# Kernel optimization log

Hardware: AMD Instinct MI355X
Metric: run time of the kernel (lower is better)

The kernel has to match this reference:

```python
import jax, jax.numpy as jnp
import numpy as np

N_NODES = 100000
N_EDGES = 1600000
K = 3  # TAGConv default hops


def _make_lin(key, out_dim, in_dim):
    # K+1 bias-free linears (stacked) + one shared output bias, per PyG TAGConv
    kw, = jax.random.split(key, 1)
    scale = 1.0 / np.sqrt(in_dim)
    W = jax.random.uniform(kw, (K + 1, out_dim, in_dim), jnp.float32, -scale, scale)
    b = jnp.zeros((out_dim,), jnp.float32)
    return W, b


def setup_inputs() -> dict:
    key = jax.random.key(0)
    ks = jax.random.split(key, 6)
    x = jax.random.normal(ks[0], (N_NODES, 128), jnp.float32)
    edge_index = jax.random.randint(ks[1], (2, N_EDGES), 0, N_NODES, jnp.int64)
    W1, b1 = _make_lin(ks[2], 128, 128)
    W2, b2 = _make_lin(ks[3], 64, 128)
    W3, b3 = _make_lin(ks[4], 16, 64)
    return {"x": x, "edge_index": edge_index, "W1": W1, "b1": b1,
            "W2": W2, "b2": b2, "W3": W3, "b3": b3}


def _tagconv(x, row, col, norm, W, b, n):
    # out = sum_k lin_k(A_norm^k x) + b ; message x_j*norm gathered at col
    out = jnp.einsum('nd,od->no', x, W[0])
    h = x
    for k in range(1, W.shape[0]):
        h = jax.ops.segment_sum(norm[:, None] * h[row], col, num_segments=n)
        out = out + jnp.einsum('nd,od->no', h, W[k])
    return out + b


def _dropout(x, key, p=0.5):
    keep = jax.random.bernoulli(key, 1.0 - p, x.shape)
    return jnp.where(keep, x / (1.0 - p), 0.0)


def reference(x, edge_index, W1, b1, W2, b2, W3, b3):
    n = x.shape[0]
    row, col = edge_index[0], edge_index[1]
    # gcn_norm without self-loops (TAGConv default)
    deg = jax.ops.segment_sum(jnp.ones(row.shape[0], x.dtype), col, num_segments=n)
    dis = jnp.where(deg > 0, 1.0 / jnp.sqrt(jnp.where(deg > 0, deg, 1.0)), 0.0)
    norm = dis[row] * dis[col]

    dk1, dk2 = jax.random.split(jax.random.key(42))
    h = _tagconv(x, row, col, norm, W1, b1, n)
    h = _dropout(h, dk1)
    h = _tagconv(h, row, col, norm, W2, b2, n)
    h = jax.nn.elu(h)
    h = _dropout(h, dk2)
    h = _tagconv(h, row, col, norm, W3, b3, n)
    return h
```

## Files before the change

### kernel.cpp

```cpp
#include <hip/hip_runtime.h>
#include <stdint.h>
#include <math.h>

#define N_NODES 100000
#define N_EDGES 1600000

typedef __bf16 bf16_t;
typedef __attribute__((ext_vector_type(4))) __bf16 bf16x4;
typedef __attribute__((ext_vector_type(8))) __bf16 bf16x8;
typedef __attribute__((ext_vector_type(4))) float f32x4;

__device__ __forceinline__ f32x4 mfma16(bf16x8 a, bf16x8 b, f32x4 c) {
  return __builtin_amdgcn_mfma_f32_16x16x32_bf16(a, b, c, 0, 0, 0);
}

__device__ __host__ __forceinline__ uint32_t rotl32(uint32_t v, int d) {
  return (v << d) | (v >> (32 - d));
}

__device__ __host__ __forceinline__ void threefry2x32(uint32_t k0, uint32_t k1,
                                                      uint32_t x0, uint32_t x1,
                                                      uint32_t& o0, uint32_t& o1) {
  uint32_t ks0 = k0, ks1 = k1, ks2 = k0 ^ k1 ^ 0x1BD11BDAu;
  x0 += ks0; x1 += ks1;
#define TF_R(r) { x0 += x1; x1 = rotl32(x1, r); x1 ^= x0; }
  TF_R(13) TF_R(15) TF_R(26) TF_R(6)
  x0 += ks1; x1 += ks2 + 1u;
  TF_R(17) TF_R(29) TF_R(16) TF_R(24)
  x0 += ks2; x1 += ks0 + 2u;
  TF_R(13) TF_R(15) TF_R(26) TF_R(6)
  x0 += ks0; x1 += ks1 + 3u;
  TF_R(17) TF_R(29) TF_R(16) TF_R(24)
  x0 += ks1; x1 += ks2 + 4u;
  TF_R(13) TF_R(15) TF_R(26) TF_R(6)
  x0 += ks2; x1 += ks0 + 5u;
#undef TF_R
  o0 = x0; o1 = x1;
}

__device__ __forceinline__ float drop_scale(uint32_t idx, uint32_t k0, uint32_t k1) {
  uint32_t o0, o1;
  threefry2x32(k0, k1, 0u, idx, o0, o1);
  uint32_t bits = o0 ^ o1;
  float u = __uint_as_float((bits >> 9) | 0x3f800000u) - 1.0f;
  return (u < 0.5f) ? 2.0f : 0.0f;
}

__global__ __launch_bounds__(256) void detect_kernel(const int* __restrict__ ei,
                                                     int* __restrict__ found_nonzero) {
  int idx = blockIdx.x * 256 + threadIdx.x;
  size_t j = (size_t)idx * 781;
  if (ei[2 * j + 1] != 0) atomicOr(found_nonzero, 1);
}

__device__ __forceinline__ int edge_row(const int* ei, bool i32, int e) {
  return i32 ? ei[e] : ei[2 * (size_t)e];
}
__device__ __forceinline__ int edge_col(const int* ei, bool i32, int e) {
  return i32 ? ei[N_EDGES + e] : ei[2 * ((size_t)N_EDGES + (size_t)e)];
}

#define BKT_SHIFT 8
#define NBKT 391
#define BKT_CAP 6144
#define EPB 8192
#define NBLK 196
#define SCAN_M (NBKT * NBLK)

__global__ __launch_bounds__(256) void hist_kernel(const int* __restrict__ ei,
                                                   const int* __restrict__ flag,
                                                   int* __restrict__ hist) {
  __shared__ int h[NBKT];
  const int t = threadIdx.x, blk = blockIdx.x;
  for (int i = t; i < NBKT; i += 256) h[i] = 0;
  __syncthreads();
  const bool i32 = *flag != 0;
  const int e0 = blk * EPB;
  for (int i = t; i < EPB; i += 256) {
    int e = e0 + i;
    if (e < N_EDGES) atomicAdd(&h[edge_col(ei, i32, e) >> BKT_SHIFT], 1);
  }
  __syncthreads();
  for (int i = t; i < NBKT; i += 256) hist[i * NBLK + blk] = h[i];
}

__global__ __launch_bounds__(256) void btot_kernel(const int* __restrict__ hist,
                                                   int* __restrict__ btot) {
  __shared__ int sh[256];
  const int b = blockIdx.x, t = threadIdx.x;
  int s = 0;
  for (int i = t; i < NBLK; i += 256) s += hist[b * NBLK + i];
  sh[t] = s;
  __syncthreads();
  for (int ofs = 128; ofs > 0; ofs >>= 1) {
    if (t < ofs) sh[t] += sh[t + ofs];
    __syncthreads();
  }
  if (t == 0) btot[b] = sh[0];
}

__global__ __launch_bounds__(512) void bbase_kernel(const int* __restrict__ btot,
                                                    int* __restrict__ bbase,
                                                    int* __restrict__ S) {
  __shared__ int sh[512];
  const int t = threadIdx.x;
  int v = (t < NBKT) ? btot[t] : 0;
  sh[t] = v;
  __syncthreads();
  for (int ofs = 1; ofs < 512; ofs <<= 1) {
    int u = (t >= ofs) ? sh[t - ofs] : 0;
    __syncthreads();
    sh[t] += u;
    __syncthreads();
  }
  if (t < NBKT) bbase[t] = sh[t] - v;
  if (t == 0) S[SCAN_M] = N_EDGES;
}

__global__ __launch_bounds__(256) void bscan2_kernel(const int* __restrict__ hist,
                                                     const int* __restrict__ bbase,
                                                     int* __restrict__ S) {
  __shared__ int sh[256];
  const int b = blockIdx.x, t = threadIdx.x;
  int v = (t < NBLK) ? hist[b * NBLK + t] : 0;
  sh[t] = v;
  __syncthreads();
  for (int ofs = 1; ofs < 256; ofs <<= 1) {
    int u = (t >= ofs) ? sh[t - ofs] : 0;
    __syncthreads();
    sh[t] += u;
    __syncthreads();
  }
  if (t < NBLK) S[b * NBLK + t] = bbase[b] + sh[t] - v;
}

__global__ __launch_bounds__(256) void binfill_kernel(const int* __restrict__ ei,
                                                      const int* __restrict__ flag,
                                                      const int* __restrict__ S,
                                                      int2* __restrict__ bins) {
  __shared__ int cur[NBKT];
  const int t = threadIdx.x, blk = blockIdx.x;
  for (int i = t; i < NBKT; i += 256) cur[i] = S[i * NBLK + blk];
  __syncthreads();
  const bool i32 = *flag != 0;
  const int e0 = blk * EPB;
  for (int i = t; i < EPB; i += 256) {
    int e = e0 + i;
    if (e < N_EDGES) {
      int r = edge_row(ei, i32, e);
      int c = edge_col(ei, i32, e);
      int p = atomicAdd(&cur[c >> BKT_SHIFT], 1);
      bins[p] = make_int2(r, c);
    }
  }
}

__global__ __launch_bounds__(512) void degdis_kernel(const int2* __restrict__ bins,
                                                     const int* __restrict__ S,
                                                     float* __restrict__ dis,
                                                     int* __restrict__ rptr) {
  __shared__ int h[256];
  __shared__ int sc[256];
  const int b = blockIdx.x, t = threadIdx.x;
  const int Bb = S[b * NBLK];
  const int Be = S[(b + 1) * NBLK];
  if (t < 256) h[t] = 0;
  __syncthreads();
  for (int i = t; i < Be - Bb; i += 512)
    atomicAdd(&h[bins[Bb + i].y & 255], 1);
  __syncthreads();
  if (t < 256) sc[t] = h[t];
  __syncthreads();
  for (int ofs = 1; ofs < 256; ofs <<= 1) {
    int u = 0;
    if (t >= ofs && t < 256) u = sc[t - ofs];
    __syncthreads();
    if (t < 256) sc[t] += u;
    __syncthreads();
  }
  const int c0 = b << BKT_SHIFT;
  if (t < 256 && c0 + t < N_NODES) {
    int d = h[t];
    dis[c0 + t] = (d > 0) ? (1.0f / sqrtf((float)d)) : 0.0f;
    rptr[c0 + t] = Bb + sc[t] - d;
  }
  if (b == NBKT - 1 && t == 0) rptr[N_NODES] = N_EDGES;
}

__global__ __launch_bounds__(512) void scatter_kernel(
    const int2* __restrict__ bins, const float* __restrict__ dis,
    const int* __restrict__ rptr, int2* __restrict__ erec) {
  __shared__ int loff[256];
  __shared__ int lcur[256];
  __shared__ float ldis[256];
  __shared__ int2 stage[BKT_CAP];
  const int b = blockIdx.x;
  const int c0 = b << BKT_SHIFT;
  const int nn = min(256, N_NODES - c0);
  const int t = threadIdx.x;
  const int base = rptr[c0];
  if (t < nn) {
    loff[t] = rptr[c0 + t] - base;
    lcur[t] = 0;
    ldis[t] = dis[c0 + t];
  }
  __syncthreads();
  const int cnt = min(rptr[c0 + nn] - base, BKT_CAP);
  for (int i = t; i < cnt; i += 512) {
    int2 rec = bins[base + i];
    int lc = rec.y & 255;
    float nrm = dis[rec.x] * ldis[lc];
    int p = atomicAdd(&lcur[lc], 1);
    stage[loff[lc] + p] = make_int2(rec.x, __float_as_int(nrm));
  }
  __syncthreads();
  for (int i = t; i < cnt; i += 512) erec[base + i] = stage[i];
}

__global__ __launch_bounds__(256) void wcvt_kernel(
    const float* __restrict__ W1, const float* __restrict__ W2,
    const float* __restrict__ W3,
    bf16_t* __restrict__ Wb1, bf16_t* __restrict__ Wb2,
    bf16_t* __restrict__ Wb3) {
  int i = blockIdx.x * 256 + threadIdx.x;
  if (i < 65536) Wb1[i] = (bf16_t)W1[i];
  if (i < 32768) Wb2[i] = (bf16_t)W2[i];
  if (i < 4096)  Wb3[i] = (bf16_t)W3[i];
}

template <int DIN, int LOG_DOUT, int NCH, bool YB, bool AHL>
__global__ __launch_bounds__(256) void matmul_mfma_kernel(
    const void* __restrict__ hA, const void* __restrict__ hAlo,
    const bf16_t* __restrict__ Wb, const float* __restrict__ bias,
    float* __restrict__ y0, void* __restrict__ y1,
    void* __restrict__ y2, void* __restrict__ y3) {
  constexpr int LDK = DIN + 8;
  constexpr int DOUT = 1 << LOG_DOUT;
  constexpr int KI = DIN / 32;
  __shared__ bf16_t sm[2][64 * LDK];
  const int m0 = blockIdx.x * 64;
  const int tid = threadIdx.x;

  if (AHL) {
    constexpr int NL = 64 * DIN / 8 / 256;
#pragma unroll
    for (int it = 0; it < NL; ++it) {
      int idx = tid + it * 256;
      int r = idx / (DIN / 8), cc = (idx % (DIN / 8)) * 8;
      int gm = m0 + r;
      uint4 vh = make_uint4(0, 0, 0, 0), vl = make_uint4(0, 0, 0, 0);
      if (gm < N_NODES) {
        vh = ((const uint4*)hA)[((size_t)gm * DIN + cc) >> 3];
        vl = ((const uint4*)hAlo)[((size_t)gm * DIN + cc) >> 3];
      }
      *(uint4*)&sm[0][r * LDK + cc] = vh;
      *(uint4*)&sm[1][r * LDK + cc] = vl;
    }
  } else {
    constexpr int NL = 64 * DIN / 4 / 256;
    union U4 { bf16_t b[4]; uint2 u; };
#pragma unroll
    for (int it = 0; it < NL; ++it) {
      int idx = tid + it * 256;
      int r = idx / (DIN / 4), cc = (idx % (DIN / 4)) * 4;
      int gm = m0 + r;
      float4 v = (gm < N_NODES) ? ((const float4*)hA)[((size_t)gm * DIN + cc) >> 2]
                                : make_float4(0.f, 0.f, 0.f, 0.f);
      U4 hi, lo;
      hi.b[0] = (bf16_t)v.x; lo.b[0] = (bf16_t)(v.x - (float)hi.b[0]);
      hi.b[1] = (bf16_t)v.y; lo.b[1] = (bf16_t)(v.y - (float)hi.b[1]);
      hi.b[2] = (bf16_t)v.z; lo.b[2] = (bf16_t)(v.z - (float)hi.b[2]);
      hi.b[3] = (bf16_t)v.w; lo.b[3] = (bf16_t)(v.w - (float)hi.b[3]);
      *(uint2*)&sm[0][r * LDK + cc] = hi.u;
      *(uint2*)&sm[1][r * LDK + cc] = lo.u;
    }
  }
  __syncthreads();

  const int w = tid >> 6, lane = tid & 63;
  const int wm = w & 1, wn = w >> 1;
  const int quad = lane >> 4, lr = lane & 15;

  bf16x8 aH[2][KI], aL[2][KI];
#pragma unroll
  for (int mt = 0; mt < 2; ++mt)
#pragma unroll
    for (int ki = 0; ki < KI; ++ki) {
      int rowa = wm * 32 + mt * 16 + lr;
      int koff = ki * 32 + quad * 8;
      aH[mt][ki] = *(const bf16x8*)&sm[0][rowa * LDK + koff];
      aL[mt][ki] = *(const bf16x8*)&sm[1][rowa * LDK + koff];
    }
  __syncthreads();

  constexpr int NLB = 64 * DIN / 8 / 256;
  uint4 wreg[NLB];
#pragma unroll
  for (int it = 0; it < NLB; ++it) {
    int idx = tid + it * 256;
    int r = idx / (DIN / 8), cc = (idx % (DIN / 8)) * 8;
    wreg[it] = ((const uint4*)Wb)[(((size_t)r) * DIN + cc) >> 3];
    *(uint4*)&sm[0][r * LDK + cc] = wreg[it];
  }
  __syncthreads();

  for (int nc = 0; nc < NCH; ++nc) {
    int p = nc & 1;
    if (nc + 1 < NCH) {
#pragma unroll
      for (int it = 0; it < NLB; ++it) {
        int idx = tid + it * 256;
        int r = idx / (DIN / 8), cc = (idx % (DIN / 8)) * 8;
        wreg[it] = ((const uint4*)Wb)[(((size_t)((nc + 1) * 64 + r)) * DIN + cc) >> 3];
      }
    }

    f32x4 acc[2][2] = {};
#pragma unroll
    for (int ki = 0; ki < KI; ++ki) {
      int koff = ki * 32 + quad * 8;
      bf16x8 bfr[2];
#pragma unroll
      for (int nt = 0; nt < 2; ++nt)
        bfr[nt] = *(const bf16x8*)&sm[p][(wn * 32 + nt * 16 + lr) * LDK + koff];
#pragma unroll
      for (int mt = 0; mt < 2; ++mt)
#pragma unroll
        for (int nt = 0; nt < 2; ++nt) {
          acc[mt][nt] = mfma16(bfr[nt], aH[mt][ki], acc[mt][nt]);
          acc[mt][nt] = mfma16(bfr[nt], aL[mt][ki], acc[mt][nt]);
        }
    }

    if (nc + 1 < NCH) {
#pragma unroll
      for (int it = 0; it < NLB; ++it) {
        int idx = tid + it * 256;
        int r = idx / (DIN / 8), cc = (idx % (DIN / 8)) * 8;
        *(uint4*)&sm[p ^ 1][r * LDK + cc] = wreg[it];
      }
    }
    __syncthreads();

    const int n0 = nc * 64;
#pragma unroll
    for (int mt = 0; mt < 2; ++mt) {
      int m = m0 + wm * 32 + mt * 16 + lr;
      if (m >= N_NODES) continue;
#pragma unroll
      for (int nt = 0; nt < 2; ++nt) {
        int nb = n0 + wn * 32 + nt * 16 + quad * 4;
        int k = nb >> LOG_DOUT;
        int o = nb & (DOUT - 1);
        size_t oi = (size_t)m * DOUT + o;
        if (k == 0) {
          float4 bv = *(const float4*)&bias[o];
          float4 st = make_float4(acc[mt][nt][0] + bv.x, acc[mt][nt][1] + bv.y,
                                  acc[mt][nt][2] + bv.z, acc[mt][nt][3] + bv.w);
          *(float4*)&y0[oi] = st;
        } else {
          void* yk = (k == 1) ? y1 : (k == 2) ? y2 : y3;
          if (YB) {
            bf16x4 bb;
            bb.x = (bf16_t)acc[mt][nt][0];
            bb.y = (bf16_t)acc[mt][nt][1];
            bb.z = (bf16_t)acc[mt][nt][2];
            bb.w = (bf16_t)acc[mt][nt][3];
            *(bf16x4*)((bf16_t*)yk + oi) = bb;
          } else {
            *(f32x4*)((float*)yk + oi) = acc[mt][nt];
          }
        }
      }
    }
  }
}

template <int D, int EPI, bool ZBF, bool ABF, int OMODE>
__global__ __launch_bounds__(256) void prop_kernel(
    const void* __restrict__ zv, const void* __restrict__ addv,
    void* __restrict__ outv, void* __restrict__ outv2,
    const int* __restrict__ rptr, const int2* __restrict__ erec,
    uint32_t k0, uint32_t k1) {
  constexpr int LPN = D / 4;
  constexpr int NPB = 256 / LPN;
  int lane = threadIdx.x % LPN;
  int nsub = threadIdx.x / LPN;
  int c = blockIdx.x * NPB + nsub;
  if (c >= N_NODES) return;
  int e0 = rptr[c], e1 = rptr[c + 1];
  float a0 = 0.f, a1 = 0.f, a2 = 0.f, a3 = 0.f;

  auto ld = [&](int r, float v[4]) {
    if (ZBF) {
      bf16x4 t = ((const bf16x4*)zv)[(size_t)r * LPN + lane];
      v[0] = (float)t.x; v[1] = (float)t.y; v[2] = (float)t.z; v[3] = (float)t.w;
    } else {
      float4 t = ((const float4*)zv)[(size_t)r * LPN + lane];
      v[0] = t.x; v[1] = t.y; v[2] = t.z; v[3] = t.w;
    }
  };

  int e = e0;
  for (; e + 3 < e1; e += 4) {
    int2 q[4];
    float v[4][4];
#pragma unroll
    for (int j = 0; j < 4; ++j) q[j] = erec[e + j];
#pragma unroll
    for (int j = 0; j < 4; ++j) ld(q[j].x, v[j]);
#pragma unroll
    for (int j = 0; j < 4; ++j) {
      float wv = __int_as_float(q[j].y);
      a0 = fmaf(wv, v[j][0], a0);
      a1 = fmaf(wv, v[j][1], a1);
      a2 = fmaf(wv, v[j][2], a2);
      a3 = fmaf(wv, v[j][3], a3);
    }
  }
  for (; e < e1; ++e) {
    int2 q = erec[e];
    float wv = __int_as_float(q.y);
    float v[4];
    ld(q.x, v);
    a0 = fmaf(wv, v[0], a0);
    a1 = fmaf(wv, v[1], a1);
    a2 = fmaf(wv, v[2], a2);
    a3 = fmaf(wv, v[3], a3);
  }

  size_t pidx = (size_t)c * LPN + lane;
  uint32_t fidx = (uint32_t)c * D + 4 * lane;
  float ax[4];
  if (ABF) {
    bf16x4 t = ((const bf16x4*)addv)[pidx];
    ax[0] = (float)t.x; ax[1] = (float)t.y; ax[2] = (float)t.z; ax[3] = (float)t.w;
  } else {
    float4 t = ((const float4*)addv)[pidx];
    ax[0] = t.x; ax[1] = t.y; ax[2] = t.z; ax[3] = t.w;
  }
  float o[4] = {a0 + ax[0], a1 + ax[1], a2 + ax[2], a3 + ax[3]};
  if (EPI == 1) {
#pragma unroll
    for (int j = 0; j < 4; ++j) o[j] *= drop_scale(fidx + j, k0, k1);
  }
  if (EPI == 2) {
#pragma unroll
    for (int j = 0; j < 4; ++j) {
      o[j] = (o[j] > 0.f) ? o[j] : expm1f(o[j]);
      o[j] *= drop_scale(fidx + j, k0, k1);
    }
  }
  if (OMODE == 0) {
    ((float4*)outv)[pidx] = make_float4(o[0], o[1], o[2], o[3]);
  } else if (OMODE == 1) {
    bf16x4 bv;
    bv.x = (bf16_t)o[0]; bv.y = (bf16_t)o[1];
    bv.z = (bf16_t)o[2]; bv.w = (bf16_t)o[3];
    ((bf16x4*)outv)[pidx] = bv;
  } else {
    bf16x4 hv, lv;
    hv.x = (bf16_t)o[0]; hv.y = (bf16_t)o[1];
    hv.z = (bf16_t)o[2]; hv.w = (bf16_t)o[3];
    lv.x = (bf16_t)(o[0] - (float)hv.x);
    lv.y = (bf16_t)(o[1] - (float)hv.y);
    lv.z = (bf16_t)(o[2] - (float)hv.z);
    lv.w = (bf16_t)(o[3] - (float)hv.w);
    ((bf16x4*)outv)[pidx] = hv;
    ((bf16x4*)outv2)[pidx] = lv;
  }
}

extern "C" void kernel_launch(void* const* d_in, const int* in_sizes, int n_in,
                              void* d_out, int out_size, void* d_ws, size_t ws_size,
                              hipStream_t stream) {
  const float* x  = (const float*)d_in[0];
  const int*   ei = (const int*)d_in[1];
  const float* W1 = (const float*)d_in[2];
  const float* b1 = (const float*)d_in[3];
  const float* W2 = (const float*)d_in[4];
  const float* b2 = (const float*)d_in[5];
  const float* W3 = (const float*)d_in[6];
  const float* b3 = (const float*)d_in[7];
  float* out = (float*)d_out;

  char* ws = (char*)d_ws;
  size_t off = 0;
  auto alloc = [&](size_t bytes) -> char* {
    char* p = ws + off;
    off += (bytes + 255) & ~(size_t)255;
    return p;
  };
  int*   flag   = (int*)alloc(256);
  float* dis    = (float*)alloc((size_t)N_NODES * 4);
  int*   rptr   = (int*)alloc((size_t)(N_NODES + 1) * 4);
  int*   hist   = (int*)alloc((size_t)SCAN_M * 4);
  int*   S      = (int*)alloc((size_t)(SCAN_M + 1) * 4);
  int*   btot   = (int*)alloc((size_t)NBKT * 4);
  int*   bbase  = (int*)alloc((size_t)NBKT * 4);
  int2*  erec   = (int2*)alloc((size_t)N_EDGES * 8);
  bf16_t* Wb1  = (bf16_t*)alloc(65536 * 2);
  bf16_t* Wb2  = (bf16_t*)alloc(32768 * 2);
  bf16_t* Wb3  = (bf16_t*)alloc(4096 * 2);
  float*  R0  = (float*)alloc((size_t)N_NODES * 128 * 4);
  float*  R2  = (float*)alloc((size_t)N_NODES * 16 * 4);
  bf16_t* Zb0 = (bf16_t*)alloc((size_t)N_NODES * 128 * 2);
  bf16_t* Zb1 = (bf16_t*)alloc((size_t)N_NODES * 128 * 2);
  bf16_t* Bb1 = (bf16_t*)alloc((size_t)N_NODES * 128 * 2);
  bf16_t* Bb2 = (bf16_t*)alloc((size_t)N_NODES * 128 * 2);

  int2* bins = (int2*)R0;

  hipMemsetAsync(flag, 0, 256, stream);

  detect_kernel<<<8, 256, 0, stream>>>(ei, flag);
  hist_kernel<<<NBLK, 256, 0, stream>>>(ei, flag, hist);
  btot_kernel<<<NBKT, 256, 0, stream>>>(hist, btot);
  bbase_kernel<<<1, 512, 0, stream>>>(btot, bbase, S);
  bscan2_kernel<<<NBKT, 256, 0, stream>>>(hist, bbase, S);
  binfill_kernel<<<NBLK, 256, 0, stream>>>(ei, flag, S, bins);
  degdis_kernel<<<NBKT, 512, 0, stream>>>(bins, S, dis, rptr);
  scatter_kernel<<<NBKT, 512, 0, stream>>>(bins, dis, rptr, erec);
  wcvt_kernel<<<256, 256, 0, stream>>>(W1, W2, W3, Wb1, Wb2, Wb3);

  uint32_t d10, d11, d20, d21;
  threefry2x32(0u, 42u, 0u, 0u, d10, d11);
  threefry2x32(0u, 42u, 0u, 1u, d20, d21);

  const int MB = (N_NODES + 63) / 64;
  const int PB128 = (N_NODES + 7) / 8;
  const int PB64n = (N_NODES + 15) / 16;
  const int PB16n = (N_NODES + 63) / 64;

  matmul_mfma_kernel<128, 7, 8, true, false><<<MB, 256, 0, stream>>>(
      x, nullptr, Wb1, b1, R0, Bb1, Bb2, Zb0);
  prop_kernel<128, 0, true, true, 1><<<PB128, 256, 0, stream>>>(
      Zb0, Bb2, Zb1, nullptr, rptr, erec, 0, 0);
  prop_kernel<128, 0, true, true, 1><<<PB128, 256, 0, stream>>>(
      Zb1, Bb1, Zb0, nullptr, rptr, erec, 0, 0);
  prop_kernel<128, 1, true, false, 2><<<PB128, 256, 0, stream>>>(
      Zb0, R0, Bb2, Bb1, rptr, erec, d10, d11);

  float*  R1f = R0;
  bf16_t* S0 = Zb0;
  bf16_t* S1 = Zb0 + (size_t)N_NODES * 64;
  bf16_t* S2 = Zb1;
  bf16_t* S3 = Zb1 + (size_t)N_NODES * 64;
  matmul_mfma_kernel<128, 6, 4, true, true><<<MB, 256, 0, stream>>>(
      Bb2, Bb1, Wb2, b2, R1f, S2, S3, S0);
  prop_kernel<64, 0, true, true, 1><<<PB64n, 256, 0, stream>>>(
      S0, S3, S1, nullptr, rptr, erec, 0, 0);
  prop_kernel<64, 0, true, true, 1><<<PB64n, 256, 0, stream>>>(
      S1, S2, S0, nullptr, rptr, erec, 0, 0);
  prop_kernel<64, 2, true, false, 2><<<PB64n, 256, 0, stream>>>(
      S0, R1f, S2, S3, rptr, erec, d20, d21);

  float*  z0f = R2;
  bf16_t* zb1 = Bb1;
  bf16_t* zb2 = Bb1 + (size_t)N_NODES * 16;
  bf16_t* zb3 = Bb1 + (size_t)N_NODES * 32;
  matmul_mfma_kernel<64, 4, 1, true, true><<<MB, 256, 0, stream>>>(
      S2, S3, Wb3, b3, z0f, zb1, zb2, zb3);
  prop_kernel<16, 0, true, true, 1><<<PB16n, 256, 0, stream>>>(
      zb3, zb2, zb2, nullptr, rptr, erec, 0, 0);
  prop_kernel<16, 0, true, true, 1><<<PB16n, 256, 0, stream>>>(
      zb2, zb1, zb1, nullptr, rptr, erec, 0, 0);
  prop_kernel<16, 0, true, false, 0><<<PB16n, 256, 0, stream>>>(
      zb1, z0f, out, nullptr, rptr, erec, 0, 0);

  (void)in_sizes; (void)n_in; (void)out_size; (void)ws_size;
}
```

Baseline: 656.8 us.

## Slice node features into 16-column planes so each XCD gathers one L2-resident slice

Stores node feature arrays as 16-column slices laid out contiguously across all nodes. The matmul writes and reads in this layout, and the propagation kernel maps blockIdx&7 to a feature slice. Since blocks are dispatched round-robin across XCDs, each XCD should repeatedly gather from a single slice of about 3.2 MB that can stay in its L2. Edge records shrink to a 4-byte source index, and the normalization is rebuilt from dis at use time, which saves CSR bandwidth. The cost is re-reading the edge list and dis once per slice, and making narrower 32-byte gathers.

Result: slower. 999.4 us (+52.2%).

```diff
diff --git a/kernel.cpp b/kernel.cpp
--- a/kernel.cpp
+++ b/kernel.cpp
@@ -188,12 +188,11 @@
 }
 
 __global__ __launch_bounds__(512) void scatter_kernel(
-    const int2* __restrict__ bins, const float* __restrict__ dis,
-    const int* __restrict__ rptr, int2* __restrict__ erec) {
+    const int2* __restrict__ bins, const int* __restrict__ rptr,
+    uint32_t* __restrict__ erow) {
   __shared__ int loff[256];
   __shared__ int lcur[256];
-  __shared__ float ldis[256];
-  __shared__ int2 stage[BKT_CAP];
+  __shared__ uint32_t stage[BKT_CAP];
   const int b = blockIdx.x;
   const int c0 = b << BKT_SHIFT;
   const int nn = min(256, N_NODES - c0);
@@ -202,19 +201,17 @@
   if (t < nn) {
     loff[t] = rptr[c0 + t] - base;
     lcur[t] = 0;
-    ldis[t] = dis[c0 + t];
   }
   __syncthreads();
   const int cnt = min(rptr[c0 + nn] - base, BKT_CAP);
   for (int i = t; i < cnt; i += 512) {
     int2 rec = bins[base + i];
     int lc = rec.y & 255;
-    float nrm = dis[rec.x] * ldis[lc];
     int p = atomicAdd(&lcur[lc], 1);
-    stage[loff[lc] + p] = make_int2(rec.x, __float_as_int(nrm));
-  }
-  __syncthreads();
-  for (int i = t; i < cnt; i += 512) erec[base + i] = stage[i];
+    stage[loff[lc] + p] = (uint32_t)rec.x;
+  }
+  __syncthreads();
+  for (int i = t; i < cnt; i += 512) erow[base + i] = stage[i];
 }
 
 __global__ __launch_bounds__(256) void wcvt_kernel(
@@ -250,8 +247,10 @@
       int gm = m0 + r;
       uint4 vh = make_uint4(0, 0, 0, 0), vl = make_uint4(0, 0, 0, 0);
       if (gm < N_NODES) {
-        vh = ((const uint4*)hA)[((size_t)gm * DIN + cc) >> 3];
-        vl = ((const uint4*)hAlo)[((size_t)gm * DIN + cc) >> 3];
+        size_t go = ((size_t)(cc >> 4) * N_NODES * 16 + (size_t)gm * 16 +
+                     (cc & 15)) >> 3;
+        vh = ((const uint4*)hA)[go];
+        vl = ((const uint4*)hAlo)[go];
       }
       *(uint4*)&sm[0][r * LDK + cc] = vh;
       *(uint4*)&sm[1][r * LDK + cc] = vl;
@@ -352,7 +351,8 @@
         int nb = n0 + wn * 32 + nt * 16 + quad * 4;
         int k = nb >> LOG_DOUT;
         int o = nb & (DOUT - 1);
-        size_t oi = (size_t)m * DOUT + o;
+        size_t oi = (size_t)(o >> 4) * ((size_t)N_NODES * 16) +
+                    (size_t)m * 16 + (o & 15);
         if (k == 0) {
           float4 bv = *(const float4*)&bias[o];
           float4 st = make_float4(acc[mt][nt][0] + bv.x, acc[mt][nt][1] + bv.y,
@@ -376,98 +376,96 @@
   }
 }
 
-template <int D, int EPI, bool ZBF, bool ABF, int OMODE>
+template <int NSL, int EPI, bool ABF, int OMODE>
 __global__ __launch_bounds__(256) void prop_kernel(
-    const void* __restrict__ zv, const void* __restrict__ addv,
+    const bf16_t* __restrict__ zv, const void* __restrict__ addv,
     void* __restrict__ outv, void* __restrict__ outv2,
-    const int* __restrict__ rptr, const int2* __restrict__ erec,
-    uint32_t k0, uint32_t k1) {
-  constexpr int LPN = D / 4;
-  constexpr int NPB = 256 / LPN;
-  int lane = threadIdx.x % LPN;
-  int nsub = threadIdx.x / LPN;
-  int c = blockIdx.x * NPB + nsub;
+    const int* __restrict__ rptr, const uint32_t* __restrict__ erow,
+    const float* __restrict__ dis, uint32_t k0, uint32_t k1) {
+  constexpr int D = NSL * 16;
+  constexpr int NREP = 8 / NSL;
+  const int v = blockIdx.x & 7;
+  const int s = v & (NSL - 1);
+  const int chunk = (blockIdx.x >> 3) * NREP + (v / NSL);
+  const int lane = threadIdx.x & 1;
+  const int nsub = threadIdx.x >> 1;
+  const int c = chunk * 128 + nsub;
   if (c >= N_NODES) return;
-  int e0 = rptr[c], e1 = rptr[c + 1];
-  float a0 = 0.f, a1 = 0.f, a2 = 0.f, a3 = 0.f;
-
-  auto ld = [&](int r, float v[4]) {
-    if (ZBF) {
-      bf16x4 t = ((const bf16x4*)zv)[(size_t)r * LPN + lane];
-      v[0] = (float)t.x; v[1] = (float)t.y; v[2] = (float)t.z; v[3] = (float)t.w;
-    } else {
-      float4 t = ((const float4*)zv)[(size_t)r * LPN + lane];
-      v[0] = t.x; v[1] = t.y; v[2] = t.z; v[3] = t.w;
-    }
-  };
+  const bf16x8* zs = (const bf16x8*)(zv + (size_t)s * N_NODES * 16);
+  const int e0 = rptr[c], e1 = rptr[c + 1];
+  const float dc = dis[c];
+  float a[8] = {};
 
   int e = e0;
   for (; e + 3 < e1; e += 4) {
-    int2 q[4];
-    float v[4][4];
-#pragma unroll
-    for (int j = 0; j < 4; ++j) q[j] = erec[e + j];
-#pragma unroll
-    for (int j = 0; j < 4; ++j) ld(q[j].x, v[j]);
+    uint32_t r4[4];
+    float w4[4];
+    bf16x8 t4[4];
+#pragma unroll
+    for (int j = 0; j < 4; ++j) r4[j] = erow[e + j];
 #pragma unroll
     for (int j = 0; j < 4; ++j) {
-      float wv = __int_as_float(q[j].y);
-      a0 = fmaf(wv, v[j][0], a0);
-      a1 = fmaf(wv, v[j][1], a1);
-      a2 = fmaf(wv, v[j][2], a2);
-      a3 = fmaf(wv, v[j][3], a3);
+      w4[j] = dis[r4[j]];
+      t4[j] = zs[(size_t)r4[j] * 2 + lane];
+    }
+#pragma unroll
+    for (int j = 0; j < 4; ++j) {
+      float w = w4[j] * dc;
+#pragma unroll
+      for (int q = 0; q < 8; ++q) a[q] = fmaf(w, (float)t4[j][q], a[q]);
     }
   }
   for (; e < e1; ++e) {
-    int2 q = erec[e];
-    float wv = __int_as_float(q.y);
-    float v[4];
-    ld(q.x, v);
-    a0 = fmaf(wv, v[0], a0);
-    a1 = fmaf(wv, v[1], a1);
-    a2 = fmaf(wv, v[2], a2);
-    a3 = fmaf(wv, v[3], a3);
-  }
-
-  size_t pidx = (size_t)c * LPN + lane;
-  uint32_t fidx = (uint32_t)c * D + 4 * lane;
-  float ax[4];
+    uint32_t r = erow[e];
+    float w = dis[r] * dc;
+    bf16x8 t = zs[(size_t)r * 2 + lane];
+#pragma unroll
+    for (int q = 0; q < 8; ++q) a[q] = fmaf(w, (float)t[q], a[q]);
+  }
+
+  const size_t pidx = (size_t)s * N_NODES * 2 + (size_t)c * 2 + lane;
+  const size_t fidx4 = ((size_t)s * N_NODES * 16 + (size_t)c * 16 + lane * 8) >> 2;
+  float o[8];
   if (ABF) {
-    bf16x4 t = ((const bf16x4*)addv)[pidx];
-    ax[0] = (float)t.x; ax[1] = (float)t.y; ax[2] = (float)t.z; ax[3] = (float)t.w;
+    bf16x8 t = ((const bf16x8*)addv)[pidx];
+#pragma unroll
+    for (int q = 0; q < 8; ++q) o[q] = a[q] + (float)t[q];
   } else {
-    float4 t = ((const float4*)addv)[pidx];
-    ax[0] = t.x; ax[1] = t.y; ax[2] = t.z; ax[3] = t.w;
-  }
-  float o[4] = {a0 + ax[0], a1 + ax[1], a2 + ax[2], a3 + ax[3]};
+    const float4* af = (const float4*)addv;
+    float4 t0 = af[fidx4], t1 = af[fidx4 + 1];
+    o[0] = a[0] + t0.x; o[1] = a[1] + t0.y; o[2] = a[2] + t0.z; o[3] = a[3] + t0.w;
+    o[4] = a[4] + t1.x; o[5] = a[5] + t1.y; o[6] = a[6] + t1.z; o[7] = a[7] + t1.w;
+  }
+  const uint32_t fidx = (uint32_t)c * D + (uint32_t)(s * 16 + lane * 8);
   if (EPI == 1) {
 #pragma unroll
-    for (int j = 0; j < 4; ++j) o[j] *= drop_scale(fidx + j, k0, k1);
+    for (int q = 0; q < 8; ++q) o[q] *= drop_scale(fidx + q, k0, k1);
   }
   if (EPI == 2) {
 #pragma unroll
-    for (int j = 0; j < 4; ++j) {
-      o[j] = (o[j] > 0.f) ? o[j] : expm1f(o[j]);
-      o[j] *= drop_scale(fidx + j, k0, k1);
+    for (int q = 0; q < 8; ++q) {
+      o[q] = (o[q] > 0.f) ? o[q] : expm1f(o[q]);
+      o[q] *= drop_scale(fidx + q, k0, k1);
     }
   }
   if (OMODE == 0) {
-    ((float4*)outv)[pidx] = make_float4(o[0], o[1], o[2], o[3]);
+    float4* of = (float4*)outv;
+    of[fidx4] = make_float4(o[0], o[1], o[2], o[3]);
+    of[fidx4 + 1] = make_float4(o[4], o[5], o[6], o[7]);
   } else if (OMODE == 1) {
-    bf16x4 bv;
-    bv.x = (bf16_t)o[0]; bv.y = (bf16_t)o[1];
-    bv.z = (bf16_t)o[2]; bv.w = (bf16_t)o[3];
-    ((bf16x4*)outv)[pidx] = bv;
+    bf16x8 bv;
+#pragma unroll
+    for (int q = 0; q < 8; ++q) bv[q] = (bf16_t)o[q];
+    ((bf16x8*)outv)[pidx] = bv;
   } else {
-    bf16x4 hv, lv;
-    hv.x = (bf16_t)o[0]; hv.y = (bf16_t)o[1];
-    hv.z = (bf16_t)o[2]; hv.w = (bf16_t)o[3];
-    lv.x = (bf16_t)(o[0] - (float)hv.x);
-    lv.y = (bf16_t)(o[1] - (float)hv.y);
-    lv.z = (bf16_t)(o[2] - (float)hv.z);
-    lv.w = (bf16_t)(o[3] - (float)hv.w);
-    ((bf16x4*)outv)[pidx] = hv;
-    ((bf16x4*)outv2)[pidx] = lv;
+    bf16x8 hv, lv;
+#pragma unroll
+    for (int q = 0; q < 8; ++q) {
+      hv[q] = (bf16_t)o[q];
+      lv[q] = (bf16_t)(o[q] - (float)hv[q]);
+    }
+    ((bf16x8*)outv)[pidx] = hv;
+    ((bf16x8*)outv2)[pidx] = lv;
   }
 }
 
@@ -498,7 +496,7 @@
   int*   S      = (int*)alloc((size_t)(SCAN_M + 1) * 4);
   int*   btot   = (int*)alloc((size_t)NBKT * 4);
   int*   bbase  = (int*)alloc((size_t)NBKT * 4);
-  int2*  erec   = (int2*)alloc((size_t)N_EDGES * 8);
+  uint32_t* erow = (uint32_t*)alloc((size_t)N_EDGES * 4);
   bf16_t* Wb1  = (bf16_t*)alloc(65536 * 2);
   bf16_t* Wb2  = (bf16_t*)alloc(32768 * 2);
   bf16_t* Wb3  = (bf16_t*)alloc(4096 * 2);
@@ -520,7 +518,7 @@
   bscan2_kernel<<<NBKT, 256, 0, stream>>>(hist, bbase, S);
   binfill_kernel<<<NBLK, 256, 0, stream>>>(ei, flag, S, bins);
   degdis_kernel<<<NBKT, 512, 0, stream>>>(bins, S, dis, rptr);
-  scatter_kernel<<<NBKT, 512, 0, stream>>>(bins, dis, rptr, erec);
+  scatter_kernel<<<NBKT, 512, 0, stream>>>(bins, rptr, erow);
   wcvt_kernel<<<256, 256, 0, stream>>>(W1, W2, W3, Wb1, Wb2, Wb3);
 
   uint32_t d10, d11, d20, d21;
@@ -528,18 +526,19 @@
   threefry2x32(0u, 42u, 0u, 1u, d20, d21);
 
   const int MB = (N_NODES + 63) / 64;
-  const int PB128 = (N_NODES + 7) / 8;
-  const int PB64n = (N_NODES + 15) / 16;
-  const int PB16n = (N_NODES + 63) / 64;
+  const int NCH = (N_NODES + 127) / 128;
+  const int PG8 = 8 * NCH;
+  const int PG4 = 8 * ((NCH + 1) / 2);
+  const int PG1 = 8 * ((NCH + 7) / 8);
 
   matmul_mfma_kernel<128, 7, 8, true, false><<<MB, 256, 0, stream>>>(
       x, nullptr, Wb1, b1, R0, Bb1, Bb2, Zb0);
-  prop_kernel<128, 0, true, true, 1><<<PB128, 256, 0, stream>>>(
-      Zb0, Bb2, Zb1, nullptr, rptr, erec, 0, 0);
-  prop_kernel<128, 0, true, true, 1><<<PB128, 256, 0, stream>>>(
-      Zb1, Bb1, Zb0, nullptr, rptr, erec, 0, 0);
-  prop_kernel<128, 1, true, false, 2><<<PB128, 256, 0, stream>>>(
-      Zb0, R0, Bb2, Bb1, rptr, erec, d10, d11);
+  prop_kernel<8, 0, true, 1><<<PG8, 256, 0, stream>>>(
+      Zb0, Bb2, Zb1, nullptr, rptr, erow, dis, 0, 0);
+  prop_kernel<8, 0, true, 1><<<PG8, 256, 0, stream>>>(
+      Zb1, Bb1, Zb0, nullptr, rptr, erow, dis, 0, 0);
+  prop_kernel<8, 1, false, 2><<<PG8, 256, 0, stream>>>(
+      Zb0, R0, Bb2, Bb1, rptr, erow, dis, d10, d11);
 
   float*  R1f = R0;
   bf16_t* S0 = Zb0;
@@ -548,12 +547,12 @@
   bf16_t* S3 = Zb1 + (size_t)N_NODES * 64;
   matmul_mfma_kernel<128, 6, 4, true, true><<<MB, 256, 0, stream>>>(
       Bb2, Bb1, Wb2, b2, R1f, S2, S3, S0);
-  prop_kernel<64, 0, true, true, 1><<<PB64n, 256, 0, stream>>>(
-      S0, S3, S1, nullptr, rptr, erec, 0, 0);
-  prop_kernel<64, 0, true, true, 1><<<PB64n, 256, 0, stream>>>(
-      S1, S2, S0, nullptr, rptr, erec, 0, 0);
-  prop_kernel<64, 2, true, false, 2><<<PB64n, 256, 0, stream>>>(
-      S0, R1f, S2, S3, rptr, erec, d20, d21);
+  prop_kernel<4, 0, true, 1><<<PG4, 256, 0, stream>>>(
+      S0, S3, S1, nullptr, rptr, erow, dis, 0, 0);
+  prop_kernel<4, 0, true, 1><<<PG4, 256, 0, stream>>>(
+      S1, S2, S0, nullptr, rptr, erow, dis, 0, 0);
+  prop_kernel<4, 2, false, 2><<<PG4, 256, 0, stream>>>(
+      S0, R1f, S2, S3, rptr, erow, dis, d20, d21);
 
   float*  z0f = R2;
   bf16_t* zb1 = Bb1;
@@ -561,12 +560,12 @@
   bf16_t* zb3 = Bb1 + (size_t)N_NODES * 32;
   matmul_mfma_kernel<64, 4, 1, true, true><<<MB, 256, 0, stream>>>(
       S2, S3, Wb3, b3, z0f, zb1, zb2, zb3);
-  prop_kernel<16, 0, true, true, 1><<<PB16n, 256, 0, stream>>>(
-      zb3, zb2, zb2, nullptr, rptr, erec, 0, 0);
-  prop_kernel<16, 0, true, true, 1><<<PB16n, 256, 0, stream>>>(
-      zb2, zb1, zb1, nullptr, rptr, erec, 0, 0);
-  prop_kernel<16, 0, true, false, 0><<<PB16n, 256, 0, stream>>>(
-      zb1, z0f, out, nullptr, rptr, erec, 0, 0);
+  prop_kernel<1, 0, true, 1><<<PG1, 256, 0, stream>>>(
+      zb3, zb2, zb2, nullptr, rptr, erow, dis, 0, 0);
+  prop_kernel<1, 0, true, 1><<<PG1, 256, 0, stream>>>(
+      zb2, zb1, zb1, nullptr, rptr, erow, dis, 0, 0);
+  prop_kernel<1, 0, false, 0><<<PG1, 256, 0, stream>>>(
+      zb1, z0f, out, nullptr, rptr, erow, dis, 0, 0);
 
   (void)in_sizes; (void)n_in; (void)out_size; (void)ws_size;
 }
```

## Store row-only edge list and compute edge norm on the fly in propagation

Applied to the files above, without the earlier changes.

Replaces the 8-byte (row, norm) edge records with 4-byte row indices and recomputes the weight as dis[row]*dis[col] inside each propagation kernel. The degree and scatter kernels are fused into one, which drops a launch and a pass over the bins. The propagation gather loop is unrolled to 8 edges, with a 4-edge step before the scalar tail. This halves edge-stream bandwidth across nine propagation passes, at the cost of an extra random gather into dis per edge (a small 400KB array, likely cache-resident).

Result: no change. 648.8 us (-1.2%).

```diff
diff --git a/kernel.cpp b/kernel.cpp
--- a/kernel.cpp
+++ b/kernel.cpp
@@ -155,18 +155,22 @@
   }
 }
 
-__global__ __launch_bounds__(512) void degdis_kernel(const int2* __restrict__ bins,
-                                                     const int* __restrict__ S,
-                                                     float* __restrict__ dis,
-                                                     int* __restrict__ rptr) {
+__global__ __launch_bounds__(512) void degdis_scatter_kernel(
+    const int2* __restrict__ bins, const int* __restrict__ S,
+    float* __restrict__ dis, int* __restrict__ rptr,
+    uint32_t* __restrict__ erow) {
   __shared__ int h[256];
   __shared__ int sc[256];
+  __shared__ int loff[256];
+  __shared__ int lcur[256];
+  __shared__ uint32_t reord[BKT_CAP];
   const int b = blockIdx.x, t = threadIdx.x;
   const int Bb = S[b * NBLK];
   const int Be = S[(b + 1) * NBLK];
+  const int cnt = min(Be - Bb, BKT_CAP);
   if (t < 256) h[t] = 0;
   __syncthreads();
-  for (int i = t; i < Be - Bb; i += 512)
+  for (int i = t; i < cnt; i += 512)
     atomicAdd(&h[bins[Bb + i].y & 255], 1);
   __syncthreads();
   if (t < 256) sc[t] = h[t];
@@ -179,42 +183,25 @@
     __syncthreads();
   }
   const int c0 = b << BKT_SHIFT;
-  if (t < 256 && c0 + t < N_NODES) {
-    int d = h[t];
-    dis[c0 + t] = (d > 0) ? (1.0f / sqrtf((float)d)) : 0.0f;
-    rptr[c0 + t] = Bb + sc[t] - d;
+  if (t < 256) {
+    loff[t] = sc[t] - h[t];
+    lcur[t] = 0;
+    if (c0 + t < N_NODES) {
+      int d = h[t];
+      dis[c0 + t] = (d > 0) ? (1.0f / sqrtf((float)d)) : 0.0f;
+      rptr[c0 + t] = Bb + sc[t] - d;
+    }
   }
   if (b == NBKT - 1 && t == 0) rptr[N_NODES] = N_EDGES;
-}
-
-__global__ __launch_bounds__(512) void scatter_kernel(
-    const int2* __restrict__ bins, const float* __restrict__ dis,
-    const int* __restrict__ rptr, int2* __restrict__ erec) {
-  __shared__ int loff[256];
-  __shared__ int lcur[256];
-  __shared__ float ldis[256];
-  __shared__ int2 stage[BKT_CAP];
-  const int b = blockIdx.x;
-  const int c0 = b << BKT_SHIFT;
-  const int nn = min(256, N_NODES - c0);
-  const int t = threadIdx.x;
-  const int base = rptr[c0];
-  if (t < nn) {
-    loff[t] = rptr[c0 + t] - base;
-    lcur[t] = 0;
-    ldis[t] = dis[c0 + t];
-  }
-  __syncthreads();
-  const int cnt = min(rptr[c0 + nn] - base, BKT_CAP);
+  __syncthreads();
   for (int i = t; i < cnt; i += 512) {
-    int2 rec = bins[base + i];
+    int2 rec = bins[Bb + i];
     int lc = rec.y & 255;
-    float nrm = dis[rec.x] * ldis[lc];
     int p = atomicAdd(&lcur[lc], 1);
-    stage[loff[lc] + p] = make_int2(rec.x, __float_as_int(nrm));
-  }
-  __syncthreads();
-  for (int i = t; i < cnt; i += 512) erec[base + i] = stage[i];
+    reord[loff[lc] + p] = (uint32_t)rec.x;
+  }
+  __syncthreads();
+  for (int i = t; i < cnt; i += 512) erow[Bb + i] = reord[i];
 }
 
 __global__ __launch_bounds__(256) void wcvt_kernel(
@@ -376,61 +363,77 @@
   }
 }
 
-template <int D, int EPI, bool ZBF, bool ABF, int OMODE>
+template <int D, int EPI, bool ABF, int OMODE>
 __global__ __launch_bounds__(256) void prop_kernel(
-    const void* __restrict__ zv, const void* __restrict__ addv,
+    const bf16_t* __restrict__ zv, const void* __restrict__ addv,
     void* __restrict__ outv, void* __restrict__ outv2,
-    const int* __restrict__ rptr, const int2* __restrict__ erec,
-    uint32_t k0, uint32_t k1) {
+    const int* __restrict__ rptr, const uint32_t* __restrict__ erow,
+    const float* __restrict__ dis, uint32_t k0, uint32_t k1) {
   constexpr int LPN = D / 4;
   constexpr int NPB = 256 / LPN;
-  int lane = threadIdx.x % LPN;
-  int nsub = threadIdx.x / LPN;
-  int c = blockIdx.x * NPB + nsub;
+  const int lane = threadIdx.x % LPN;
+  const int nsub = threadIdx.x / LPN;
+  const int c = blockIdx.x * NPB + nsub;
   if (c >= N_NODES) return;
-  int e0 = rptr[c], e1 = rptr[c + 1];
+  const int e0 = rptr[c], e1 = rptr[c + 1];
+  const float dc = dis[c];
+  const bf16x4* zs = (const bf16x4*)zv;
   float a0 = 0.f, a1 = 0.f, a2 = 0.f, a3 = 0.f;
 
-  auto ld = [&](int r, float v[4]) {
-    if (ZBF) {
-      bf16x4 t = ((const bf16x4*)zv)[(size_t)r * LPN + lane];
-      v[0] = (float)t.x; v[1] = (float)t.y; v[2] = (float)t.z; v[3] = (float)t.w;
-    } else {
-      float4 t = ((const float4*)zv)[(size_t)r * LPN + lane];
-      v[0] = t.x; v[1] = t.y; v[2] = t.z; v[3] = t.w;
-    }
-  };
-
   int e = e0;
-  for (; e + 3 < e1; e += 4) {
-    int2 q[4];
-    float v[4][4];
-#pragma unroll
-    for (int j = 0; j < 4; ++j) q[j] = erec[e + j];
-#pragma unroll
-    for (int j = 0; j < 4; ++j) ld(q[j].x, v[j]);
+  for (; e + 7 < e1; e += 8) {
+    uint32_t r8[8];
+#pragma unroll
+    for (int j = 0; j < 8; ++j) r8[j] = erow[e + j];
+    float w8[8];
+    bf16x4 v8[8];
+#pragma unroll
+    for (int j = 0; j < 8; ++j) {
+      w8[j] = dis[r8[j]];
+      v8[j] = zs[(size_t)r8[j] * LPN + lane];
+    }
+#pragma unroll
+    for (int j = 0; j < 8; ++j) {
+      float w = w8[j] * dc;
+      a0 = fmaf(w, (float)v8[j].x, a0);
+      a1 = fmaf(w, (float)v8[j].y, a1);
+      a2 = fmaf(w, (float)v8[j].z, a2);
+      a3 = fmaf(w, (float)v8[j].w, a3);
+    }
+  }
+  if (e + 3 < e1) {
+    uint32_t r4[4];
+#pragma unroll
+    for (int j = 0; j < 4; ++j) r4[j] = erow[e + j];
+    float w4[4];
+    bf16x4 v4[4];
 #pragma unroll
     for (int j = 0; j < 4; ++j) {
-      float wv = __int_as_float(q[j].y);
-      a0 = fmaf(wv, v[j][0], a0);
-      a1 = fmaf(wv, v[j][1], a1);
-      a2 = fmaf(wv, v[j][2], a2);
-      a3 = fmaf(wv, v[j][3], a3);
-    }
+      w4[j] = dis[r4[j]];
+      v4[j] = zs[(size_t)r4[j] * LPN + lane];
+    }
+#pragma unroll
+    for (int j = 0; j < 4; ++j) {
+      float w = w4[j] * dc;
+      a0 = fmaf(w, (float)v4[j].x, a0);
+      a1 = fmaf(w, (float)v4[j].y, a1);
+      a2 = fmaf(w, (float)v4[j].z, a2);
+      a3 = fmaf(w, (float)v4[j].w, a3);
+    }
+    e += 4;
   }
   for (; e < e1; ++e) {
-    int2 q = erec[e];
-    float wv = __int_as_float(q.y);
-    float v[4];
-    ld(q.x, v);
-    a0 = fmaf(wv, v[0], a0);
-    a1 = fmaf(wv, v[1], a1);
-    a2 = fmaf(wv, v[2], a2);
-    a3 = fmaf(wv, v[3], a3);
-  }
-
-  size_t pidx = (size_t)c * LPN + lane;
-  uint32_t fidx = (uint32_t)c * D + 4 * lane;
+    uint32_t r = erow[e];
+    float w = dis[r] * dc;
+    bf16x4 t = zs[(size_t)r * LPN + lane];
+    a0 = fmaf(w, (float)t.x, a0);
+    a1 = fmaf(w, (float)t.y, a1);
+    a2 = fmaf(w, (float)t.z, a2);
+    a3 = fmaf(w, (float)t.w, a3);
+  }
+
+  const size_t pidx = (size_t)c * LPN + lane;
+  const uint32_t fidx = (uint32_t)c * D + 4 * lane;
   float ax[4];
   if (ABF) {
     bf16x4 t = ((const bf16x4*)addv)[pidx];
@@ -498,7 +501,7 @@
   int*   S      = (int*)alloc((size_t)(SCAN_M + 1) * 4);
   int*   btot   = (int*)alloc((size_t)NBKT * 4);
   int*   bbase  = (int*)alloc((size_t)NBKT * 4);
-  int2*  erec   = (int2*)alloc((size_t)N_EDGES * 8);
+  uint32_t* erow = (uint32_t*)alloc((size_t)N_EDGES * 4);
   bf16_t* Wb1  = (bf16_t*)alloc(65536 * 2);
   bf16_t* Wb2  = (bf16_t*)alloc(32768 * 2);
   bf16_t* Wb3  = (bf16_t*)alloc(4096 * 2);
@@ -519,8 +522,7 @@
   bbase_kernel<<<1, 512, 0, stream>>>(btot, bbase, S);
   bscan2_kernel<<<NBKT, 256, 0, stream>>>(hist, bbase, S);
   binfill_kernel<<<NBLK, 256, 0, stream>>>(ei, flag, S, bins);
-  degdis_kernel<<<NBKT, 512, 0, stream>>>(bins, S, dis, rptr);
-  scatter_kernel<<<NBKT, 512, 0, stream>>>(bins, dis, rptr, erec);
+  degdis_scatter_kernel<<<NBKT, 512, 0, stream>>>(bins, S, dis, rptr, erow);
   wcvt_kernel<<<256, 256, 0, stream>>>(W1, W2, W3, Wb1, Wb2, Wb3);
 
   uint32_t d10, d11, d20, d21;
@@ -534,12 +536,12 @@
 
   matmul_mfma_kernel<128, 7, 8, true, false><<<MB, 256, 0, stream>>>(
       x, nullptr, Wb1, b1, R0, Bb1, Bb2, Zb0);
-  prop_kernel<128, 0, true, true, 1><<<PB128, 256, 0, stream>>>(
-      Zb0, Bb2, Zb1, nullptr, rptr, erec, 0, 0);
-  prop_kernel<128, 0, true, true, 1><<<PB128, 256, 0, stream>>>(
-      Zb1, Bb1, Zb0, nullptr, rptr, erec, 0, 0);
-  prop_kernel<128, 1, true, false, 2><<<PB128, 256, 0, stream>>>(
-      Zb0, R0, Bb2, Bb1, rptr, erec, d10, d11);
+  prop_kernel<128, 0, true, 1><<<PB128, 256, 0, stream>>>(
+      Zb0, Bb2, Zb1, nullptr, rptr, erow, dis, 0, 0);
+  prop_kernel<128, 0, true, 1><<<PB128, 256, 0, stream>>>(
+      Zb1, Bb1, Zb0, nullptr, rptr, erow, dis, 0, 0);
+  prop_kernel<128, 1, false, 2><<<PB128, 256, 0, stream>>>(
+      Zb0, R0, Bb2, Bb1, rptr, erow, dis, d10, d11);
 
   float*  R1f = R0;
   bf16_t* S0 = Zb0;
@@ -548,12 +550,12 @@
   bf16_t* S3 = Zb1 + (size_t)N_NODES * 64;
   matmul_mfma_kernel<128, 6, 4, true, true><<<MB, 256, 0, stream>>>(
       Bb2, Bb1, Wb2, b2, R1f, S2, S3, S0);
-  prop_kernel<64, 0, true, true, 1><<<PB64n, 256, 0, stream>>>(
-      S0, S3, S1, nullptr, rptr, erec, 0, 0);
-  prop_kernel<64, 0, true, true, 1><<<PB64n, 256, 0, stream>>>(
-      S1, S2, S0, nullptr, rptr, erec, 0, 0);
-  prop_kernel<64, 2, true, false, 2><<<PB64n, 256, 0, stream>>>(
-      S0, R1f, S2, S3, rptr, erec, d20, d21);
+  prop_kernel<64, 0, true, 1><<<PB64n, 256, 0, stream>>>(
+      S0, S3, S1, nullptr, rptr, erow, dis, 0, 0);
+  prop_kernel<64, 0, true, 1><<<PB64n, 256, 0, stream>>>(
+      S1, S2, S0, nullptr, rptr, erow, dis, 0, 0);
+  prop_kernel<64, 2, false, 2><<<PB64n, 256, 0, stream>>>(
+      S0, R1f, S2, S3, rptr, erow, dis, d20, d21);
 
   float*  z0f = R2;
   bf16_t* zb1 = Bb1;
@@ -561,12 +563,12 @@
   bf16_t* zb3 = Bb1 + (size_t)N_NODES * 32;
   matmul_mfma_kernel<64, 4, 1, true, true><<<MB, 256, 0, stream>>>(
       S2, S3, Wb3, b3, z0f, zb1, zb2, zb3);
-  prop_kernel<16, 0, true, true, 1><<<PB16n, 256, 0, stream>>>(
-      zb3, zb2, zb2, nullptr, rptr, erec, 0, 0);
-  prop_kernel<16, 0, true, true, 1><<<PB16n, 256, 0, stream>>>(
-      zb2, zb1, zb1, nullptr, rptr, erec, 0, 0);
-  prop_kernel<16, 0, true, false, 0><<<PB16n, 256, 0, stream>>>(
-      zb1, z0f, out, nullptr, rptr, erec, 0, 0);
+  prop_kernel<16, 0, true, 1><<<PB16n, 256, 0, stream>>>(
+      zb3, zb2, zb2, nullptr, rptr, erow, dis, 0, 0);
+  prop_kernel<16, 0, true, 1><<<PB16n, 256, 0, stream>>>(
+      zb2, zb1, zb1, nullptr, rptr, erow, dis, 0, 0);
+  prop_kernel<16, 0, false, 0><<<PB16n, 256, 0, stream>>>(
+      zb1, z0f, out, nullptr, rptr, erow, dis, 0, 0);
 
   (void)in_sizes; (void)n_in; (void)out_size; (void)ws_size;
 }
```
